# Optimization experiments

Hardware: AMD Instinct MI355X
Metric: run time of the kernel (lower is better)

The kernel has to match this reference:

```python
import jax, jax.numpy as jnp
import numpy as np

TARGET_KAPPA = 1.0 / 61.0
EPS = 1e-10

# --- antisymmetric expansion: 35 independent components (i<j<k) -> (7,7,7) ---
_combos = np.array([(i, j, k) for i in range(7) for j in range(i + 1, 7) for k in range(j + 1, 7)])  # (35,3)
_perm_specs = [((0, 1, 2), 1.0), ((0, 2, 1), -1.0), ((1, 0, 2), -1.0), ((1, 2, 0), 1.0), ((2, 0, 1), 1.0), ((2, 1, 0), -1.0)]
_I = jnp.array(np.concatenate([_combos[:, p[0]] for p, _ in _perm_specs]))
_J = jnp.array(np.concatenate([_combos[:, p[1]] for p, _ in _perm_specs]))
_K = jnp.array(np.concatenate([_combos[:, p[2]] for p, _ in _perm_specs]))
_S = jnp.array(np.concatenate([np.full(35, s, dtype=np.float32) for _, s in _perm_specs]))


def expand_to_antisymmetric(v35):
    # v35: (35,) -> antisymmetric (7,7,7)
    vals = jnp.tile(v35, 6) * _S.astype(v35.dtype)
    return jnp.zeros((7, 7, 7), v35.dtype).at[_I, _J, _K].set(vals)


def _phi_single(xi, W1, b1, W2, b2):
    # xi: (7,) -> antisymmetric 3-form (7,7,7)
    h = jnp.tanh(xi @ W1 + b1)          # (H,)
    v35 = h @ W2 + b2                    # (35,)
    return expand_to_antisymmetric(v35)


def setup_inputs() -> dict:
    key = jax.random.key(0)
    k1, k2, k3 = jax.random.split(key, 3)
    B, H = 32768, 512
    x = jax.random.normal(k1, (B, 7), dtype=jnp.float32)
    W1 = jax.random.normal(k2, (7, H), dtype=jnp.float32) * 0.3
    b1 = jnp.zeros((H,), dtype=jnp.float32)
    W2 = jax.random.normal(k3, (H, 35), dtype=jnp.float32) * 0.05
    b2 = jnp.zeros((35,), dtype=jnp.float32)
    return {"x": x, "W1": W1, "b1": b1, "W2": W2, "b2": b2}


def reference(x, W1, b1, W2, b2):
    f = lambda xi: _phi_single(xi, W1, b1, W2, b2)
    # Jacobian replaces the 35 looped autograd.grad calls: (B,7,7,7,7), last axis = d/dx_l
    jac = jax.vmap(jax.jacfwd(f))(x)
    d_phi = jnp.moveaxis(jac, -1, 1)  # (B, 7(deriv), 7, 7, 7), matching torch layout
    torsion_sq = jnp.sum(d_phi ** 2, axis=(1, 2, 3, 4))  # (B,)
    torsion_norm = jnp.sqrt(torsion_sq + EPS)
    loss = jnp.mean((torsion_norm - TARGET_KAPPA) ** 2)
    return loss, jnp.mean(torsion_norm)
```

## Files before the change

kernel.cpp:

```cpp
#include <hip/hip_runtime.h>
#include <hip/hip_bf16.h>
#include <math.h>

typedef __attribute__((ext_vector_type(8)))  short bf16x8;
typedef __attribute__((ext_vector_type(16))) float f32x16;
typedef unsigned int u32;

#define KAPPA (1.0f/61.0f)
#define NBLK 512

__device__ __forceinline__ unsigned short f2bf(float f) {
    u32 x = __float_as_uint(f);
    x += 0x7fffu + ((x >> 16) & 1u);
    return (unsigned short)(x >> 16);
}
__device__ __forceinline__ float fast_rcp(float v) {
#if __has_builtin(__builtin_amdgcn_rcpf)
    return __builtin_amdgcn_rcpf(v);
#else
    return 1.0f / v;
#endif
}
__device__ __forceinline__ u32 pack_bf16(float lo, float hi) {
    __hip_bfloat162 p = __float22bfloat162_rn(make_float2(lo, hi));
    return *reinterpret_cast<u32*>(&p);
}

__global__ void build_v(const float* __restrict__ W1, const float* __restrict__ W2,
                        const float* __restrict__ b1,
                        bf16x8* __restrict__ V, bf16x8* __restrict__ Wt) {
    int t = blockIdx.x * blockDim.x + threadIdx.x;
    if (t < 16384) {
        int lane = t & 63, ptile = (t >> 6) & 7, kkg = t >> 9;
        int p  = ptile * 32 + (lane & 31);
        int hb = kkg * 16 + (lane >> 5) * 8;
        bool valid = (p < 245);
        int l7 = valid ? p / 35 : 0;
        int c  = valid ? p - l7 * 35 : 0;
        bf16x8 v;
#pragma unroll
        for (int i = 0; i < 8; ++i) {
            int h = hb + i;
            v[i] = valid ? (short)f2bf(W1[l7 * 512 + h] * W2[h * 35 + c]) : (short)0;
        }
        V[t] = v;
    } else if (t < 16384 + 1024) {
        int f = t - 16384;
        int lane = f & 63, htile = f >> 6;
        int h = htile * 32 + (lane & 31);
        bf16x8 v;
#pragma unroll
        for (int i = 0; i < 8; ++i) v[i] = 0;
        if (lane < 32) {
#pragma unroll
            for (int l = 0; l < 7; ++l) v[l] = (short)f2bf(W1[l * 512 + h]);
            v[7] = (short)f2bf(b1[h]);
        }
        Wt[f] = v;
    }
}

__global__ __launch_bounds__(512, 4)
void torsion_main(const float* __restrict__ x,
                  const bf16x8* __restrict__ V, const bf16x8* __restrict__ Wt,
                  float* __restrict__ partials) {
    __shared__ __align__(16) u32 Gb[2][16][64 * 4];
    __shared__ float red[4][2][32];

    const int tid  = threadIdx.x;
    const int lane = tid & 63;
    const int w    = tid >> 6;
    const int st   = w & 1;
    const int pp   = w >> 1;
    const int blk  = blockIdx.x;

    bf16x8 xf;
#pragma unroll
    for (int i = 0; i < 8; ++i) xf[i] = 0;
    if (lane < 32) {
        const float* xp = x + ((size_t)blk * 64 + st * 32 + lane) * 7;
#pragma unroll
        for (int l = 0; l < 7; ++l) xf[l] = (short)f2bf(xp[l]);
        xf[7] = (short)f2bf(1.0f);
    }

    f32x16 acc[2];
#pragma unroll
    for (int pt = 0; pt < 2; ++pt)
#pragma unroll
        for (int e = 0; e < 16; ++e) acc[pt][e] = 0.0f;

    auto pre_pack = [&](int c, u32 d[8]) {
        bf16x8 wf = Wt[(c * 4 + pp) * 64 + lane];
        f32x16 p;
#pragma unroll
        for (int e = 0; e < 16; ++e) p[e] = 0.0f;
        p = __builtin_amdgcn_mfma_f32_32x32x16_bf16(wf, xf, p, 0, 0, 0);
#pragma unroll
        for (int j = 0; j < 8; ++j) {
            float t0 = __expf(-2.0f * fabsf(p[2 * j]));
            float r0 = fast_rcp(1.0f + t0);
            float g0 = 4.0f * t0 * r0 * r0;
            float t1 = __expf(-2.0f * fabsf(p[2 * j + 1]));
            float r1 = fast_rcp(1.0f + t1);
            float g1 = 4.0f * t1 * r1 * r1;
            d[j] = pack_bf16(g0, g1);
        }
    };
    auto store_g = [&](int buf, const u32 d[8]) {
        const int f0  = 4 * pp + st;
        const int f1  = f0 + 2;
        const int col = lane & 31;
        const int hw2 = (lane >> 5) << 1;
        *reinterpret_cast<uint2*>(&Gb[buf][f0][(col     ) * 4 + hw2]) = make_uint2(d[0], d[1]);
        *reinterpret_cast<uint2*>(&Gb[buf][f0][(col + 32) * 4 + hw2]) = make_uint2(d[2], d[3]);
        *reinterpret_cast<uint2*>(&Gb[buf][f1][(col     ) * 4 + hw2]) = make_uint2(d[4], d[5]);
        *reinterpret_cast<uint2*>(&Gb[buf][f1][(col + 32) * 4 + hw2]) = make_uint2(d[6], d[7]);
    };

    {
        u32 d0[8];
        pre_pack(0, d0);
        store_g(0, d0);
    }
    __syncthreads();

    for (int c = 0; c < 4; ++c) {
        const int buf = c & 1;
        u32 dn[8];
        if (c < 3) pre_pack(c + 1, dn);
        __builtin_amdgcn_s_setprio(1);
#pragma unroll
        for (int ks = 0; ks < 8; ++ks) {
            bf16x8 g = *reinterpret_cast<const bf16x8*>(&Gb[buf][ks * 2 + st][lane * 4]);
            const int fb = ((c * 8 + ks) * 8 + 2 * pp) * 64 + lane;
            bf16x8 va = V[fb];
            bf16x8 vb = V[fb + 64];
            acc[0] = __builtin_amdgcn_mfma_f32_32x32x16_bf16(va, g, acc[0], 0, 0, 0);
            acc[1] = __builtin_amdgcn_mfma_f32_32x32x16_bf16(vb, g, acc[1], 0, 0, 0);
        }
        __builtin_amdgcn_s_setprio(0);
        if (c < 3) store_g(buf ^ 1, dn);
        __syncthreads();
    }

    {
        float s = 0.0f;
#pragma unroll
        for (int pt = 0; pt < 2; ++pt)
#pragma unroll
            for (int e = 0; e < 16; ++e) s += acc[pt][e] * acc[pt][e];
        s += __shfl_xor(s, 32);
        if (lane < 32) red[pp][st][lane] = s;
    }
    __syncthreads();

    if (tid < 64) {
        const int col = tid & 31, ss = tid >> 5;
        float q = 6.0f * (red[0][ss][col] + red[1][ss][col] + red[2][ss][col] + red[3][ss][col]);
        float n = sqrtf(q + 1e-10f);
        float d = n - KAPPA;
        float a = d * d, b = n;
#pragma unroll
        for (int m = 1; m <= 32; m <<= 1) {
            a += __shfl_xor(a, m);
            b += __shfl_xor(b, m);
        }
        if (tid == 0) {
            partials[blk]        = a;
            partials[NBLK + blk] = b;
        }
    }
}

__global__ void finalize_k(const float* __restrict__ partials, float* __restrict__ out) {
    __shared__ float sl[256], sn[256];
    int tid = threadIdx.x;
    sl[tid] = partials[tid] + partials[tid + 256];
    sn[tid] = partials[NBLK + tid] + partials[NBLK + tid + 256];
    __syncthreads();
    for (int st = 128; st > 0; st >>= 1) {
        if (tid < st) { sl[tid] += sl[tid + st]; sn[tid] += sn[tid + st]; }
        __syncthreads();
    }
    if (tid == 0) {
        out[0] = sl[0] / 32768.0f;
        out[1] = sn[0] / 32768.0f;
    }
}

extern "C" void kernel_launch(void* const* d_in, const int* in_sizes, int n_in,
                              void* d_out, int out_size, void* d_ws, size_t ws_size,
                              hipStream_t stream) {
    const float* x  = (const float*)d_in[0];
    const float* W1 = (const float*)d_in[1];
    const float* b1 = (const float*)d_in[2];
    const float* W2 = (const float*)d_in[3];

    bf16x8* V        = (bf16x8*)d_ws;
    bf16x8* Wt       = V + 16384;
    float*  partials = (float*)(Wt + 1024);

    build_v<<<68, 256, 0, stream>>>(W1, W2, b1, V, Wt);
    torsion_main<<<NBLK, 512, 0, stream>>>(x, V, Wt, partials);
    finalize_k<<<1, 256, 0, stream>>>(partials, (float*)d_out);
}
```

Baseline: 28.96 us.

## Split output columns across two blocks per sample tile to double grid size

Each 64-sample tile is now handled by two 256-thread blocks, each computing half of the 245 output rows (ph selects the row half). Per-sample partial squared norms are written to a 2x32768 buffer, and the sqrt/loss step moves into a single 1024-thread finalize kernel. The aim is more blocks for better CU occupancy and load balance on the MI355X. The cost is that the tanh-derivative (G) computation is repeated in both blocks, the partials buffer is larger, and the single-block finalize now reads 64K floats.

```diff
diff --git a/kernel.cpp b/kernel.cpp
--- a/kernel.cpp
+++ b/kernel.cpp
@@ -7,7 +7,7 @@
 typedef unsigned int u32;
 
 #define KAPPA (1.0f/61.0f)
-#define NBLK 512
+#define NBLK 1024
 
 __device__ __forceinline__ unsigned short f2bf(float f) {
     u32 x = __float_as_uint(f);
@@ -60,25 +60,26 @@
     }
 }
 
-__global__ __launch_bounds__(512, 4)
+__global__ __launch_bounds__(256, 4)
 void torsion_main(const float* __restrict__ x,
                   const bf16x8* __restrict__ V, const bf16x8* __restrict__ Wt,
                   float* __restrict__ partials) {
-    __shared__ __align__(16) u32 Gb[2][16][64 * 4];
-    __shared__ float red[4][2][32];
+    __shared__ __align__(16) u32 Gb[2][8][64 * 4];
+    __shared__ float red[2][64];
 
     const int tid  = threadIdx.x;
     const int lane = tid & 63;
     const int w    = tid >> 6;
     const int st   = w & 1;
-    const int pp   = w >> 1;
-    const int blk  = blockIdx.x;
+    const int hp   = w >> 1;
+    const int sblk = blockIdx.x >> 1;
+    const int ph   = blockIdx.x & 1;
 
     bf16x8 xf;
 #pragma unroll
     for (int i = 0; i < 8; ++i) xf[i] = 0;
     if (lane < 32) {
-        const float* xp = x + ((size_t)blk * 64 + st * 32 + lane) * 7;
+        const float* xp = x + ((size_t)sblk * 64 + st * 32 + lane) * 7;
 #pragma unroll
         for (int l = 0; l < 7; ++l) xf[l] = (short)f2bf(xp[l]);
         xf[7] = (short)f2bf(1.0f);
@@ -91,7 +92,7 @@
         for (int e = 0; e < 16; ++e) acc[pt][e] = 0.0f;
 
     auto pre_pack = [&](int c, u32 d[8]) {
-        bf16x8 wf = Wt[(c * 4 + pp) * 64 + lane];
+        bf16x8 wf = Wt[(c * 2 + hp) * 64 + lane];
         f32x16 p;
 #pragma unroll
         for (int e = 0; e < 16; ++e) p[e] = 0.0f;
@@ -108,7 +109,7 @@
         }
     };
     auto store_g = [&](int buf, const u32 d[8]) {
-        const int f0  = 4 * pp + st;
+        const int f0  = 4 * hp + st;
         const int f1  = f0 + 2;
         const int col = lane & 31;
         const int hw2 = (lane >> 5) << 1;
@@ -125,22 +126,22 @@
     }
     __syncthreads();
 
-    for (int c = 0; c < 4; ++c) {
+    for (int c = 0; c < 8; ++c) {
         const int buf = c & 1;
         u32 dn[8];
-        if (c < 3) pre_pack(c + 1, dn);
+        if (c < 7) pre_pack(c + 1, dn);
         __builtin_amdgcn_s_setprio(1);
 #pragma unroll
-        for (int ks = 0; ks < 8; ++ks) {
+        for (int ks = 0; ks < 4; ++ks) {
             bf16x8 g = *reinterpret_cast<const bf16x8*>(&Gb[buf][ks * 2 + st][lane * 4]);
-            const int fb = ((c * 8 + ks) * 8 + 2 * pp) * 64 + lane;
+            const int fb = ((c * 4 + ks) * 8 + ph * 4 + 2 * hp) * 64 + lane;
             bf16x8 va = V[fb];
             bf16x8 vb = V[fb + 64];
             acc[0] = __builtin_amdgcn_mfma_f32_32x32x16_bf16(va, g, acc[0], 0, 0, 0);
             acc[1] = __builtin_amdgcn_mfma_f32_32x32x16_bf16(vb, g, acc[1], 0, 0, 0);
         }
         __builtin_amdgcn_s_setprio(0);
-        if (c < 3) store_g(buf ^ 1, dn);
+        if (c < 7) store_g(buf ^ 1, dn);
         __syncthreads();
     }
 
@@ -151,35 +152,30 @@
 #pragma unroll
             for (int e = 0; e < 16; ++e) s += acc[pt][e] * acc[pt][e];
         s += __shfl_xor(s, 32);
-        if (lane < 32) red[pp][st][lane] = s;
+        if (lane < 32) red[hp][st * 32 + lane] = s;
     }
     __syncthreads();
 
     if (tid < 64) {
-        const int col = tid & 31, ss = tid >> 5;
-        float q = 6.0f * (red[0][ss][col] + red[1][ss][col] + red[2][ss][col] + red[3][ss][col]);
+        partials[(size_t)ph * 32768 + sblk * 64 + tid] = red[0][tid] + red[1][tid];
+    }
+}
+
+__global__ __launch_bounds__(1024)
+void finalize_k(const float* __restrict__ partials, float* __restrict__ out) {
+    __shared__ float sl[1024], sn[1024];
+    const int tid = threadIdx.x;
+    float a = 0.0f, b = 0.0f;
+    for (int s = tid; s < 32768; s += 1024) {
+        float q = 6.0f * (partials[s] + partials[32768 + s]);
         float n = sqrtf(q + 1e-10f);
         float d = n - KAPPA;
-        float a = d * d, b = n;
-#pragma unroll
-        for (int m = 1; m <= 32; m <<= 1) {
-            a += __shfl_xor(a, m);
-            b += __shfl_xor(b, m);
-        }
-        if (tid == 0) {
-            partials[blk]        = a;
-            partials[NBLK + blk] = b;
-        }
-    }
-}
-
-__global__ void finalize_k(const float* __restrict__ partials, float* __restrict__ out) {
-    __shared__ float sl[256], sn[256];
-    int tid = threadIdx.x;
-    sl[tid] = partials[tid] + partials[tid + 256];
-    sn[tid] = partials[NBLK + tid] + partials[NBLK + tid + 256];
+        a += d * d;
+        b += n;
+    }
+    sl[tid] = a; sn[tid] = b;
     __syncthreads();
-    for (int st = 128; st > 0; st >>= 1) {
+    for (int st = 512; st > 0; st >>= 1) {
         if (tid < st) { sl[tid] += sl[tid + st]; sn[tid] += sn[tid + st]; }
         __syncthreads();
     }
@@ -202,6 +198,6 @@
     float*  partials = (float*)(Wt + 1024);
 
     build_v<<<68, 256, 0, stream>>>(W1, W2, b1, V, Wt);
-    torsion_main<<<NBLK, 512, 0, stream>>>(x, V, Wt, partials);
-    finalize_k<<<1, 256, 0, stream>>>(partials, (float*)d_out);
-}
+    torsion_main<<<NBLK, 256, 0, stream>>>(x, V, Wt, partials);
+    finalize_k<<<1, 1024, 0, stream>>>(partials, (float*)d_out);
+}
```

Result: slower. 44.14 us (+52.4%).
